# Kernel optimization log

Hardware: AMD Instinct MI355X
Metric: run time of the kernel (lower is better)

## Reference

```python
import jax, jax.numpy as jnp
import numpy as np
import math
from jax import lax

S = 2048   # layer_size (number of neurons)
T = 384    # timesteps per forward call
ALPHA = 0.15
DT = 0.1
THRESH = -50.0
V_RESET = -70.0
VL = -70.0
GL = 0.025
CM = 0.5
TAU = CM / GL                                   # 20.0
COEF = DT ** ALPHA * math.gamma(2.0 - ALPHA) / CM  # dt^alpha * Gamma(2-alpha) / Cm


def setup_inputs() -> dict:
    key = jax.random.key(0)
    I_old = jax.random.normal(key, (S, T), dtype=jnp.float32)
    # class-level fractional (Grunwald-Letnikov style) weight vector, x=5000
    x = 5000
    nv = np.arange(x - 1)
    w = ((x - nv + 1) ** (1.0 - ALPHA) - (x - nv) ** (1.0 - ALPHA)).astype(np.float32)
    return {"I_old": I_old, "weights": jnp.asarray(w)}


def _forward(I_old, weights):
    S_, T_ = I_old.shape
    dtype = I_old.dtype
    # wr[a] = weights[-a]: the memory weight applied to a delta that is `a` steps old.
    # Original: np.inner(weights[-N+1:], delta_trace) pairs oldest delta with weights[-(N-1)]
    # and the newest delta with weights[-1].
    wr = jnp.concatenate([jnp.zeros((1,), dtype), weights[::-1][:T_].astype(dtype)])  # [T+1]
    jidx = jnp.arange(T_)  # buffer slot j holds the delta appended at global step j

    def step(carry, xs):
        V, buf = carry          # V: [S], buf: [S, T] delta history (slot j = delta of step j)
        n, I_n = xs             # n: scalar step index, I_n: [S]
        # fractional memory term: sum_{j=1}^{n-1} wr[n-j] * delta_j
        ages = n - jidx                                        # [T]
        coeff = jnp.where((ages >= 1) & (jidx >= 1),
                          wr[jnp.clip(ages, 0, T_)], jnp.zeros((), dtype))  # [T]
        memory = buf @ coeff                                   # [S]
        # three update rules depending on the global step counter
        V1 = V + (DT / TAU) * (-V + I_n / GL)                  # N == 1 branch
        V2 = COEF * (-GL * (V - VL) + I_n) + V - memory        # N >= 2 branch
        V_pre = jnp.where(n == 0, jnp.full_like(V, -70.0),
                          jnp.where(n == 1, V1, V2))
        spike = (V - THRESH > 0).astype(dtype)                 # spike uses PREVIOUS V
        reset = lax.stop_gradient(spike * (THRESH - V_RESET))  # detached reset
        V_new = V_pre - reset
        buf = buf.at[:, n].set(V_new - V)                      # append delta (n=0 slot masked out)
        return (V_new, buf), (spike, V_new)

    V0 = jnp.zeros((S_,), dtype)          # V_trace initialized to 0 per neuron
    buf0 = jnp.zeros((S_, T_), dtype)
    (_, _), (spk, trc) = lax.scan(step, (V0, buf0), (jnp.arange(T_), I_old.T))
    return spk.T, trc.T                    # each [S, T]


def reference(I_old, weights):
    return _forward(I_old, weights)
```

## Files before the change

### kernel.cpp

```cpp
#include <hip/hip_runtime.h>
#include <cmath>

#define T_STEPS 384
#define CH 64
#define NCH 6
#define WREP_STRIDE 392

__device__ __forceinline__ float readlane_f(float v, int l) {
    return __int_as_float(__builtin_amdgcn_readlane(__float_as_int(v), l));
}

__global__ __launch_bounds__(64, 2)
void flif_kernel(const float* __restrict__ I_old, const float* __restrict__ W,
                 float* __restrict__ out, float c1, float c2, float c3, int Stot)
{
    const int s    = blockIdx.x;
    const int lane = threadIdx.x;

    __shared__ __align__(16) float wrep[4 * WREP_STRIDE];
    __shared__ float ltab[2 * CH];
    __shared__ __align__(16) float dbuf[T_STEPS];

    const float* Irow = I_old + (size_t)s * T_STEPS;
    float Inext = Irow[lane];

    ltab[lane] = 0.0f;
    ltab[64 + lane] = (lane < 63) ? W[4998 - lane] : 0.0f;
    #pragma unroll
    for (int r2 = 0; r2 < 4; ++r2) {
        for (int k = lane; k < WREP_STRIDE; k += 64) {
            const int i = k + r2;
            wrep[r2 * WREP_STRIDE + k] = (i >= 1 && i <= 383) ? W[4615 + i] : 0.0f;
        }
    }
    __syncthreads();

    float* out_spk = out + (size_t)s * T_STEPS;
    float* out_trc = out + (size_t)Stot * T_STEPS + (size_t)s * T_STEPS;

    const int rsel = (-lane) & 3;
    const float* wlane = wrep + rsel * WREP_STRIDE + (384 - lane - rsel);

    float V = 0.0f;

    float wpre[8];
    #pragma unroll
    for (int k = 0; k < 8; ++k) wpre[k] = ltab[lane + 63 - k];

    for (int c = 0; c < NCH; ++c) {
        const int cb = c * CH;
        const float Ic = Inext;
        if (c + 1 < NCH) Inext = Irow[cb + CH + lane];

        float acc = 0.0f;
        const float* wp = wlane - cb;
        #pragma unroll 4
        for (int j = 0; j < cb; j += 4) {
            const float4 d4 = *reinterpret_cast<const float4*>(&dbuf[j]);
            const float4 w4 = *reinterpret_cast<const float4*>(wp + j);
            acc = fmaf(d4.x, w4.x, acc);
            acc = fmaf(d4.y, w4.y, acc);
            acc = fmaf(d4.z, w4.z, acc);
            acc = fmaf(d4.w, w4.w, acc);
        }

        float u = fmaf(c3, Ic, c2) - acc;
        const float Vs = V;
        float tc = 0.0f;

        auto step = [&](int i) {
            const float w = wpre[i & 7];
            wpre[i & 7] = ltab[lane + 63 - ((i + 8) & 63)];
            const float t  = readlane_f(u, i);
            const float r  = (V > -50.0f) ? 20.0f : 0.0f;
            const float V2 = fmaf(c1, V, t);
            const float Vn = V2 - r;
            const float d  = Vn - V;
            u = fmaf(-w, d, u);
            if (lane == i) tc = Vn;
            V = Vn;
        };

        if (c == 0) {
            {
                wpre[0] = ltab[lane + 63 - 8];
                V = -90.0f;
                if (lane == 0) tc = V;
            }
            {
                const float w = wpre[1];
                wpre[1] = ltab[lane + 63 - 9];
                const float I1 = readlane_f(Ic, 1);
                const float V1 = fmaf(0.005f, (I1 / 0.025f) - V, V);
                const float r  = (V > -50.0f) ? 20.0f : 0.0f;
                const float Vn = V1 - r;
                const float d  = Vn - V;
                u = fmaf(-w, d, u);
                if (lane == 1) tc = Vn;
                V = Vn;
            }
            #pragma unroll
            for (int i = 2; i < CH; ++i) step(i);
        } else {
            #pragma unroll
            for (int i = 0; i < CH; ++i) step(i);
        }

        float prev = __shfl_up(tc, 1);
        if (lane == 0) prev = Vs;
        const float spk = (prev > -50.0f) ? 1.0f : 0.0f;
        float d = tc - prev;
        if (c == 0 && lane == 0) d = 0.0f;
        dbuf[cb + lane] = d;
        out_spk[cb + lane] = spk;
        out_trc[cb + lane] = tc;
        __syncthreads();
    }
}

extern "C" void kernel_launch(void* const* d_in, const int* in_sizes, int n_in,
                              void* d_out, int out_size, void* d_ws, size_t ws_size,
                              hipStream_t stream) {
    const float* I = (const float*)d_in[0];
    const float* W = (const float*)d_in[1];
    float* out = (float*)d_out;
    const int S = in_sizes[0] / T_STEPS;

    const double COEF = std::pow(0.1, 0.15) * std::tgamma(1.85) / 0.5;
    const float c3 = (float)COEF;
    const float c1 = (float)(1.0 - COEF * 0.025);
    const float c2 = (float)(COEF * 0.025 * -70.0);

    flif_kernel<<<S, 64, 0, stream>>>(I, W, out, c1, c2, c3, S);
}
```

Before: 87.69 us.

## Restructure serial recurrence to shorten dependency chain and keep weights in registers

Rewrites the per-step serial recurrence so that the delta is computed as (P - w1*d_prev) + b, where b = cm1*V + reset is precomputed one step ahead. The readlane for the next step is issued early, which takes the cross-lane read and the comparison off the critical latency chain. The 64 intra-chunk weights are loaded once into a register array from a replicated shared table, replacing the rolling per-step LDS prefetch. The cost is much higher register pressure from the 64-float array, which could reduce occupancy or cause spills, plus a reordered floating-point sum.

New measurement: 86.85 us. Within noise of the previous version (-1.0%).

```diff
diff --git a/kernel.cpp b/kernel.cpp
--- a/kernel.cpp
+++ b/kernel.cpp
@@ -12,28 +12,42 @@
 
 __global__ __launch_bounds__(64, 2)
 void flif_kernel(const float* __restrict__ I_old, const float* __restrict__ W,
-                 float* __restrict__ out, float c1, float c2, float c3, int Stot)
+                 float* __restrict__ out, float cm1, float c2, float c3, int Stot)
 {
     const int s    = blockIdx.x;
     const int lane = threadIdx.x;
 
     __shared__ __align__(16) float wrep[4 * WREP_STRIDE];
-    __shared__ float ltab[2 * CH];
+    __shared__ __align__(16) float lrep[4 * 128];
     __shared__ __align__(16) float dbuf[T_STEPS];
 
     const float* Irow = I_old + (size_t)s * T_STEPS;
     float Inext = Irow[lane];
 
-    ltab[lane] = 0.0f;
-    ltab[64 + lane] = (lane < 63) ? W[4998 - lane] : 0.0f;
     #pragma unroll
-    for (int r2 = 0; r2 < 4; ++r2) {
+    for (int r = 0; r < 4; ++r) {
         for (int k = lane; k < WREP_STRIDE; k += 64) {
-            const int i = k + r2;
-            wrep[r2 * WREP_STRIDE + k] = (i >= 1 && i <= 383) ? W[4615 + i] : 0.0f;
+            const int i = k + r;
+            wrep[r * WREP_STRIDE + k] = (i >= 1 && i <= 383) ? W[4615 + i] : 0.0f;
+        }
+        for (int k = lane; k < 128; k += 64) {
+            const int x = k + r;
+            lrep[r * 128 + k] = (x >= 64 && x <= 126) ? W[5062 - x] : 0.0f;
         }
     }
     __syncthreads();
+
+    float wloc[64];
+    {
+        const int r = lane & 3;
+        const float* lp = lrep + r * 128 - r;
+        #pragma unroll
+        for (int i0 = 0; i0 < 64; i0 += 4) {
+            const float4 f = *reinterpret_cast<const float4*>(lp + (lane + 60 - i0));
+            wloc[i0 + 0] = f.w; wloc[i0 + 1] = f.z;
+            wloc[i0 + 2] = f.y; wloc[i0 + 3] = f.x;
+        }
+    }
 
     float* out_spk = out + (size_t)s * T_STEPS;
     float* out_trc = out + (size_t)Stot * T_STEPS + (size_t)s * T_STEPS;
@@ -41,11 +55,9 @@
     const int rsel = (-lane) & 3;
     const float* wlane = wrep + rsel * WREP_STRIDE + (384 - lane - rsel);
 
-    float V = 0.0f;
+    const float wr1n = -W[4998];
 
-    float wpre[8];
-    #pragma unroll
-    for (int k = 0; k < 8; ++k) wpre[k] = ltab[lane + 63 - k];
+    float V = 0.0f, d = 0.0f, b = 0.0f, P = 0.0f;
 
     for (int c = 0; c < NCH; ++c) {
         const int cb = c * CH;
@@ -68,50 +80,45 @@
         const float Vs = V;
         float tc = 0.0f;
 
-        auto step = [&](int i) {
-            const float w = wpre[i & 7];
-            wpre[i & 7] = ltab[lane + 63 - ((i + 8) & 63)];
-            const float t  = readlane_f(u, i);
-            const float r  = (V > -50.0f) ? 20.0f : 0.0f;
-            const float V2 = fmaf(c1, V, t);
-            const float Vn = V2 - r;
-            const float d  = Vn - V;
-            u = fmaf(-w, d, u);
-            if (lane == i) tc = Vn;
-            V = Vn;
+        auto body = [&](int i) {
+            const float t = fmaf(wr1n, d, P);
+            d = t + b;
+            P = readlane_f(u, (i + 1) & 63);
+            V = V + d;
+            const float rv = (V > -50.0f) ? -20.0f : 0.0f;
+            b = fmaf(cm1, V, rv);
+            u = fmaf(-wloc[i], d, u);
+            tc = (lane == i) ? V : tc;
         };
 
         if (c == 0) {
-            {
-                wpre[0] = ltab[lane + 63 - 8];
-                V = -90.0f;
-                if (lane == 0) tc = V;
-            }
-            {
-                const float w = wpre[1];
-                wpre[1] = ltab[lane + 63 - 9];
-                const float I1 = readlane_f(Ic, 1);
-                const float V1 = fmaf(0.005f, (I1 / 0.025f) - V, V);
-                const float r  = (V > -50.0f) ? 20.0f : 0.0f;
-                const float Vn = V1 - r;
-                const float d  = Vn - V;
-                u = fmaf(-w, d, u);
-                if (lane == 1) tc = Vn;
-                V = Vn;
-            }
+            V = -90.0f;
+            if (lane == 0) tc = V;
+            const float I1 = readlane_f(Ic, 1);
+            const float V1 = fmaf(0.005f, (I1 / 0.025f) - V, V);
+            const float d1 = V1 - V;
+            P = readlane_f(u, 2);
+            u = fmaf(-wloc[1], d1, u);
+            if (lane == 1) tc = V1;
+            V = V1;
+            d = d1;
+            const float rv = (V > -50.0f) ? -20.0f : 0.0f;
+            b = fmaf(cm1, V, rv);
             #pragma unroll
-            for (int i = 2; i < CH; ++i) step(i);
+            for (int i = 2; i < CH; ++i) body(i);
         } else {
+            d = 0.0f;
+            P = readlane_f(u, 0);
             #pragma unroll
-            for (int i = 0; i < CH; ++i) step(i);
+            for (int i = 0; i < CH; ++i) body(i);
         }
 
         float prev = __shfl_up(tc, 1);
         if (lane == 0) prev = Vs;
         const float spk = (prev > -50.0f) ? 1.0f : 0.0f;
-        float d = tc - prev;
-        if (c == 0 && lane == 0) d = 0.0f;
-        dbuf[cb + lane] = d;
+        float dd = tc - prev;
+        if (c == 0 && lane == 0) dd = 0.0f;
+        dbuf[cb + lane] = dd;
         out_spk[cb + lane] = spk;
         out_trc[cb + lane] = tc;
         __syncthreads();
@@ -127,9 +134,9 @@
     const int S = in_sizes[0] / T_STEPS;
 
     const double COEF = std::pow(0.1, 0.15) * std::tgamma(1.85) / 0.5;
-    const float c3 = (float)COEF;
-    const float c1 = (float)(1.0 - COEF * 0.025);
-    const float c2 = (float)(COEF * 0.025 * -70.0);
+    const float c3  = (float)COEF;
+    const float cm1 = (float)(-COEF * 0.025);
+    const float c2  = (float)(COEF * 0.025 * -70.0);
 
-    flif_kernel<<<S, 64, 0, stream>>>(I, W, out, c1, c2, c3, S);
+    flif_kernel<<<S, 64, 0, stream>>>(I, W, out, cm1, c2, c3, S);
 }
```
